# Performance work log

Measured on AMD Instinct MI355X. Metric: run time of the kernel, lower is better.

The kernel has to match this reference:

```python
import jax, jax.numpy as jnp
import numpy as np

B, H, L = 8, 256, 8192

def setup_inputs() -> dict:
    key = jax.random.key(0)
    k1, k2, k3 = jax.random.split(key, 3)
    u = jax.random.normal(k1, (B, H, L), dtype=jnp.float32)
    K = jax.random.normal(k2, (H, L), dtype=jnp.float32)
    # D ~ uniform_ring with min=max=1.0, field='real' -> random signs on unit ring
    D = jnp.where(jax.random.uniform(k3, (H,)) < 0.5, -1.0, 1.0).astype(jnp.float32)
    return {"u": u, "K": K, "D": D}

def reference(u, K, D):
    # FFT-based circular long convolution per channel: y = ifft(fft(u) * fft(K)).real
    u_s = jnp.fft.fft(u, axis=-1)            # (B,H,L) complex
    k_s = jnp.fft.fft(K, axis=-1)            # (H,L)   complex
    y = jnp.fft.ifft(u_s * k_s[None], axis=-1).real  # (B,H,L)
    y = y + D[None, :, None] * u             # skip connection D*u
    y = jnp.tanh(y)
    return y
```

## Files before the change

kernel.cpp:

```cpp
#include <hip/hip_runtime.h>
#include <math.h>


#define LL 8192
#define NT 256
#define HH 256
#define TWO_PI 6.2831853071795864f
#define CP16 0.980785280403230f
#define SP16 0.195090322016128f
#define CP8  0.92387953251129f
#define SP8  0.38268343236509f

__device__ __forceinline__ int PH(int e) { return e ^ ((e >> 4) & 15); }

__device__ __forceinline__ float fast_tanh(float x) {
    float e = __expf(2.0f * x);
    return 1.0f - 2.0f / (e + 1.0f);
}

template<int JT>
__device__ __forceinline__ void fill_pyr_cs(float c0, float s0, float Er, float Ei,
                                            float* twr, float* twi) {
    const int off = (1 << JT) - 1;
    twr[off] = c0; twi[off] = s0;
    #pragma unroll
    for (int m = 1; m < (1 << JT); ++m) {
        const float pr = twr[off + m - 1], pi = twi[off + m - 1];
        twr[off + m] = pr * Er - pi * Ei;
        twi[off + m] = pr * Ei + pi * Er;
    }
    #pragma unroll
    for (int j = JT - 1; j >= 0; --j) {
        #pragma unroll
        for (int m = 0; m < (1 << j); ++m) {
            const float a = twr[(2 << j) - 1 + m], b = twi[(2 << j) - 1 + m];
            twr[(1 << j) - 1 + m] = a * a - b * b;
            twi[(1 << j) - 1 + m] = 2.0f * a * b;
        }
    }
}
template<int JT>
__device__ __forceinline__ void fill_pyr(float ang0, float Er, float Ei,
                                         float* twr, float* twi) {
    float s, c;
    __sincosf(ang0, &s, &c);
    fill_pyr_cs<JT>(c, s, Er, Ei, twr, twi);
}

template<int R2>
__device__ __forceinline__ void dif_apply(float* xr, float* xi,
                                          const float* twr, const float* twi) {
    #pragma unroll
    for (int j = R2 - 1; j >= 0; --j) {
        #pragma unroll
        for (int q = 0; q < (1 << (R2 - 1)); ++q) {
            const int mm = q & ((1 << j) - 1);
            const int m0 = ((q >> j) << (j + 1)) | mm;
            const int m1 = m0 + (1 << j);
            const float wr = twr[(1 << j) - 1 + mm], wi = twi[(1 << j) - 1 + mm];
            const float ar = xr[m0], ai = xi[m0], br = xr[m1], bi = xi[m1];
            xr[m0] = ar + br; xi[m0] = ai + bi;
            const float dr = ar - br, di = ai - bi;
            xr[m1] = dr * wr - di * wi;
            xi[m1] = dr * wi + di * wr;
        }
    }
}
template<int R2>
__device__ __forceinline__ void dit_apply(float* xr, float* xi,
                                          const float* twr, const float* twi) {
    #pragma unroll
    for (int j = 0; j < R2; ++j) {
        #pragma unroll
        for (int q = 0; q < (1 << (R2 - 1)); ++q) {
            const int mm = q & ((1 << j) - 1);
            const int m0 = ((q >> j) << (j + 1)) | mm;
            const int m1 = m0 + (1 << j);
            const float wr = twr[(1 << j) - 1 + mm], wi = twi[(1 << j) - 1 + mm];
            const float br = xr[m1] * wr - xi[m1] * wi;
            const float bi = xr[m1] * wi + xi[m1] * wr;
            const float ar = xr[m0], ai = xi[m0];
            xr[m0] = ar + br; xi[m0] = ai + bi;
            xr[m1] = ar - br; xi[m1] = ai - bi;
        }
    }
}

__device__ __forceinline__ void fwd_A(float* xr, float* xi, int tid, float2* buf) {
    float twr[31], twi[31];
    fill_pyr<4>(-(TWO_PI / 8192.0f) * (float)tid, CP16, -SP16, twr, twi);
    dif_apply<5>(xr, xi, twr, twi);
    #pragma unroll
    for (int m = 0; m < 32; ++m) {
        buf[PH(tid + (m << 8))] = make_float2(xr[m], xi[m]);
    }
}

__device__ __forceinline__ void fwd_B(int tid, float2* buf) {
    int pa[2][16];
    float xr[2][16], xi[2][16], twr[15], twi[15];
    #pragma unroll
    for (int gg = 0; gg < 2; ++gg) {
        const int g = tid + (gg << 8);
        const int base = ((g >> 4) << 8) | (g & 15);
        #pragma unroll
        for (int m = 0; m < 16; ++m) {
            pa[gg][m] = PH(base + (m << 4));
            const float2 v = buf[pa[gg][m]];
            xr[gg][m] = v.x; xi[gg][m] = v.y;
        }
    }
    fill_pyr<3>(-(TWO_PI / 256.0f) * (float)(tid & 15), CP8, -SP8, twr, twi);
    dif_apply<4>(xr[0], xi[0], twr, twi);
    dif_apply<4>(xr[1], xi[1], twr, twi);
    #pragma unroll
    for (int gg = 0; gg < 2; ++gg) {
        #pragma unroll
        for (int m = 0; m < 16; ++m) {
            buf[pa[gg][m]] = make_float2(xr[gg][m], xi[gg][m]);
        }
    }
}

__device__ __forceinline__ void inv_B(int tid, float2* buf) {
    int pa[2][16];
    float xr[2][16], xi[2][16], twr[15], twi[15];
    #pragma unroll
    for (int gg = 0; gg < 2; ++gg) {
        const int g = tid + (gg << 8);
        const int base = ((g >> 4) << 8) | (g & 15);
        #pragma unroll
        for (int m = 0; m < 16; ++m) {
            pa[gg][m] = PH(base + (m << 4));
            const float2 v = buf[pa[gg][m]];
            xr[gg][m] = v.x; xi[gg][m] = v.y;
        }
    }
    fill_pyr<3>((TWO_PI / 256.0f) * (float)(tid & 15), CP8, SP8, twr, twi);
    dit_apply<4>(xr[0], xi[0], twr, twi);
    dit_apply<4>(xr[1], xi[1], twr, twi);
    #pragma unroll
    for (int gg = 0; gg < 2; ++gg) {
        #pragma unroll
        for (int m = 0; m < 16; ++m) {
            buf[pa[gg][m]] = make_float2(xr[gg][m], xi[gg][m]);
        }
    }
}

__global__ __launch_bounds__(NT) void kfft_kernel(const float* __restrict__ K,
                                                  const float* __restrict__ D,
                                                  float2* __restrict__ Kf) {
    __shared__ float2 buf[LL];
    const int h = blockIdx.x;
    const int tid = threadIdx.x;
    const float* Kr = K + (size_t)h * LL;
    float xr[32], xi[32];
    #pragma unroll
    for (int m = 0; m < 32; ++m) {
        xr[m] = Kr[tid + (m << 8)];
        xi[m] = 0.0f;
    }
    fwd_A(xr, xi, tid, buf);
    __syncthreads();
    fwd_B(tid, buf);
    __syncthreads();
    const float dh = D[h];
    const float invN = 1.0f / (float)LL;
    float2* outp = Kf + (size_t)h * LL;
    float twr[15], twi[15];
    fill_pyr_cs<3>(1.0f, 0.0f, CP8, -SP8, twr, twi);
    #pragma unroll
    for (int gg = 0; gg < 2; ++gg) {
        const int i0 = tid + (gg << 8);
        const int base = i0 << 4;
        float yr[16], yi[16];
        #pragma unroll
        for (int m = 0; m < 16; ++m) {
            const float2 v = buf[PH(base + m)];
            yr[m] = v.x; yi[m] = v.y;
        }
        dif_apply<4>(yr, yi, twr, twi);
        #pragma unroll
        for (int m = 0; m < 16; ++m) {
            outp[(m << 9) + i0] = make_float2((yr[m] + dh) * invN, yi[m] * invN);
        }
    }
}

__global__ __launch_bounds__(NT) void conv_kernel(const float* __restrict__ u,
                                                  const float2* __restrict__ Kf,
                                                  float* __restrict__ out) {
    __shared__ float2 buf[LL];
    const int tid = threadIdx.x;
    const int h = blockIdx.x & (HH - 1);
    const int pr_ = blockIdx.x >> 8;
    const size_t off0 = ((size_t)(pr_ * 2) * HH + h) * LL;
    const size_t off1 = off0 + (size_t)HH * LL;
    const float* u0 = u + off0;
    const float* u1 = u + off1;

    float xr[32], xi[32];
    #pragma unroll
    for (int m = 0; m < 32; ++m) {
        xr[m] = u0[tid + (m << 8)];
        xi[m] = u1[tid + (m << 8)];
    }
    fwd_A(xr, xi, tid, buf);
    __syncthreads();
    fwd_B(tid, buf);
    __syncthreads();

    {
        const float2* kf = Kf + (size_t)h * LL;
        int pc[2][16];
        float yr[2][16], yi[2][16], twr[15], twi[15];
        #pragma unroll
        for (int gg = 0; gg < 2; ++gg) {
            const int base = (tid + (gg << 8)) << 4;
            #pragma unroll
            for (int m = 0; m < 16; ++m) {
                pc[gg][m] = PH(base + m);
                const float2 v = buf[pc[gg][m]];
                yr[gg][m] = v.x; yi[gg][m] = v.y;
            }
        }
        fill_pyr_cs<3>(1.0f, 0.0f, CP8, -SP8, twr, twi);
        dif_apply<4>(yr[0], yi[0], twr, twi);
        dif_apply<4>(yr[1], yi[1], twr, twi);
        #pragma unroll
        for (int gg = 0; gg < 2; ++gg) {
            const int i0 = tid + (gg << 8);
            #pragma unroll
            for (int m = 0; m < 16; ++m) {
                const float2 w = kf[(m << 9) + i0];
                const float a = yr[gg][m], b = yi[gg][m];
                yr[gg][m] = a * w.x - b * w.y;
                yi[gg][m] = a * w.y + b * w.x;
            }
        }
        fill_pyr_cs<3>(1.0f, 0.0f, CP8, SP8, twr, twi);
        dit_apply<4>(yr[0], yi[0], twr, twi);
        dit_apply<4>(yr[1], yi[1], twr, twi);
        #pragma unroll
        for (int gg = 0; gg < 2; ++gg) {
            #pragma unroll
            for (int m = 0; m < 16; ++m) {
                buf[pc[gg][m]] = make_float2(yr[gg][m], yi[gg][m]);
            }
        }
    }
    __syncthreads();

    inv_B(tid, buf);
    __syncthreads();

    {
        float twr[31], twi[31];
        #pragma unroll
        for (int m = 0; m < 32; ++m) {
            const float2 v = buf[PH(tid + (m << 8))];
            xr[m] = v.x; xi[m] = v.y;
        }
        fill_pyr<4>((TWO_PI / 8192.0f) * (float)tid, CP16, SP16, twr, twi);
        dit_apply<5>(xr, xi, twr, twi);
    }
    float* o0 = out + off0;
    float* o1 = out + off1;
    #pragma unroll
    for (int m = 0; m < 32; ++m) {
        const int n = tid + (m << 8);
        o0[n] = fast_tanh(xr[m]);
        o1[n] = fast_tanh(xi[m]);
    }
}

extern "C" void kernel_launch(void* const* d_in, const int* in_sizes, int n_in,
                              void* d_out, int out_size, void* d_ws, size_t ws_size,
                              hipStream_t stream) {
    const float* u = (const float*)d_in[0];
    const float* K = (const float*)d_in[1];
    const float* D = (const float*)d_in[2];
    float* out = (float*)d_out;
    float2* Kf = (float2*)d_ws;

    kfft_kernel<<<dim3(HH), dim3(NT), 0, stream>>>(K, D, Kf);
    conv_kernel<<<dim3(4 * HH), dim3(NT), 0, stream>>>(u, Kf, out);
}
```

Before: 172.4 us.

## Fuse middle FFT stages per wavefront and split shared buffer into planar arrays

The middle radix-16 stages (forward B, the radix-16 C pass with pointwise multiply, and inverse B) are regrouped so each 16-lane group owns one 256-element column block. All of that work then stays inside a wavefront, and three block-wide __syncthreads between those stages are dropped. The shared buffer changes from interleaved float2 to separate real and imaginary arrays with a new XOR swizzle, which is meant to reduce bank conflicts. The frequency-domain kernel is now stored in natural contiguous order, so it is loaded as float4 and prefetched before the FFT stages. The risks are that the intra-wave shared-memory ordering relies on wavefront lockstep without explicit barriers, and that the prefetched kernel values add register pressure.

```diff
diff --git a/kernel.cpp b/kernel.cpp
--- a/kernel.cpp
+++ b/kernel.cpp
@@ -11,8 +11,9 @@
 #define CP8  0.92387953251129f
 #define SP8  0.38268343236509f
 
-__device__ __forceinline__ int PH(int e) { return e ^ ((e >> 4) & 15); }
-
+__device__ __forceinline__ int SW(int e) {
+    return e ^ ((e >> 4) & 15) ^ (((e >> 8) & 1) << 4);
+}
 __device__ __forceinline__ float fast_tanh(float x) {
     float e = __expf(2.0f * x);
     return 1.0f - 2.0f / (e + 1.0f);
@@ -86,72 +87,23 @@
     }
 }
 
-__device__ __forceinline__ void fwd_A(float* xr, float* xi, int tid, float2* buf) {
+__device__ __forceinline__ void fwd_A(float* xr, float* xi, int tid,
+                                      float* re, float* im) {
     float twr[31], twi[31];
     fill_pyr<4>(-(TWO_PI / 8192.0f) * (float)tid, CP16, -SP16, twr, twi);
     dif_apply<5>(xr, xi, twr, twi);
     #pragma unroll
     for (int m = 0; m < 32; ++m) {
-        buf[PH(tid + (m << 8))] = make_float2(xr[m], xi[m]);
-    }
-}
-
-__device__ __forceinline__ void fwd_B(int tid, float2* buf) {
-    int pa[2][16];
-    float xr[2][16], xi[2][16], twr[15], twi[15];
-    #pragma unroll
-    for (int gg = 0; gg < 2; ++gg) {
-        const int g = tid + (gg << 8);
-        const int base = ((g >> 4) << 8) | (g & 15);
-        #pragma unroll
-        for (int m = 0; m < 16; ++m) {
-            pa[gg][m] = PH(base + (m << 4));
-            const float2 v = buf[pa[gg][m]];
-            xr[gg][m] = v.x; xi[gg][m] = v.y;
-        }
-    }
-    fill_pyr<3>(-(TWO_PI / 256.0f) * (float)(tid & 15), CP8, -SP8, twr, twi);
-    dif_apply<4>(xr[0], xi[0], twr, twi);
-    dif_apply<4>(xr[1], xi[1], twr, twi);
-    #pragma unroll
-    for (int gg = 0; gg < 2; ++gg) {
-        #pragma unroll
-        for (int m = 0; m < 16; ++m) {
-            buf[pa[gg][m]] = make_float2(xr[gg][m], xi[gg][m]);
-        }
-    }
-}
-
-__device__ __forceinline__ void inv_B(int tid, float2* buf) {
-    int pa[2][16];
-    float xr[2][16], xi[2][16], twr[15], twi[15];
-    #pragma unroll
-    for (int gg = 0; gg < 2; ++gg) {
-        const int g = tid + (gg << 8);
-        const int base = ((g >> 4) << 8) | (g & 15);
-        #pragma unroll
-        for (int m = 0; m < 16; ++m) {
-            pa[gg][m] = PH(base + (m << 4));
-            const float2 v = buf[pa[gg][m]];
-            xr[gg][m] = v.x; xi[gg][m] = v.y;
-        }
-    }
-    fill_pyr<3>((TWO_PI / 256.0f) * (float)(tid & 15), CP8, SP8, twr, twi);
-    dit_apply<4>(xr[0], xi[0], twr, twi);
-    dit_apply<4>(xr[1], xi[1], twr, twi);
-    #pragma unroll
-    for (int gg = 0; gg < 2; ++gg) {
-        #pragma unroll
-        for (int m = 0; m < 16; ++m) {
-            buf[pa[gg][m]] = make_float2(xr[gg][m], xi[gg][m]);
-        }
+        const int p = SW(tid + (m << 8));
+        re[p] = xr[m]; im[p] = xi[m];
     }
 }
 
 __global__ __launch_bounds__(NT) void kfft_kernel(const float* __restrict__ K,
                                                   const float* __restrict__ D,
                                                   float2* __restrict__ Kf) {
-    __shared__ float2 buf[LL];
+    __shared__ float re[LL];
+    __shared__ float im[LL];
     const int h = blockIdx.x;
     const int tid = threadIdx.x;
     const float* Kr = K + (size_t)h * LL;
@@ -161,29 +113,57 @@
         xr[m] = Kr[tid + (m << 8)];
         xi[m] = 0.0f;
     }
-    fwd_A(xr, xi, tid, buf);
+    fwd_A(xr, xi, tid, re, im);
     __syncthreads();
-    fwd_B(tid, buf);
-    __syncthreads();
-    const float dh = D[h];
-    const float invN = 1.0f / (float)LL;
-    float2* outp = Kf + (size_t)h * LL;
-    float twr[15], twi[15];
-    fill_pyr_cs<3>(1.0f, 0.0f, CP8, -SP8, twr, twi);
-    #pragma unroll
-    for (int gg = 0; gg < 2; ++gg) {
-        const int i0 = tid + (gg << 8);
-        const int base = i0 << 4;
-        float yr[16], yi[16];
-        #pragma unroll
-        for (int m = 0; m < 16; ++m) {
-            const float2 v = buf[PH(base + m)];
-            yr[m] = v.x; yi[m] = v.y;
-        }
-        dif_apply<4>(yr, yi, twr, twi);
-        #pragma unroll
-        for (int m = 0; m < 16; ++m) {
-            outp[(m << 9) + i0] = make_float2((yr[m] + dh) * invN, yi[m] * invN);
+
+    const int lane = tid & 63, wv = tid >> 6;
+    const int q = lane & 15, qw = (lane >> 4) & 3;
+
+    {
+        float twr[15], twi[15];
+        fill_pyr<3>(-(TWO_PI / 256.0f) * (float)q, CP8, -SP8, twr, twi);
+        #pragma unroll
+        for (int r = 0; r < 2; ++r) {
+            const int c = (wv << 3) + qw + (r << 2);
+            const int base = (c << 8) + q;
+            float ar[16], ai[16];
+            #pragma unroll
+            for (int m = 0; m < 16; ++m) {
+                const int p = SW(base + (m << 4));
+                ar[m] = re[p]; ai[m] = im[p];
+            }
+            dif_apply<4>(ar, ai, twr, twi);
+            #pragma unroll
+            for (int m = 0; m < 16; ++m) {
+                const int p = SW(base + (m << 4));
+                re[p] = ar[m]; im[p] = ai[m];
+            }
+        }
+    }
+    {
+        const float dh = D[h];
+        const float invN = 1.0f / (float)LL;
+        float twr[15], twi[15];
+        fill_pyr_cs<3>(1.0f, 0.0f, CP8, -SP8, twr, twi);
+        #pragma unroll
+        for (int r = 0; r < 2; ++r) {
+            const int c = (wv << 3) + qw + (r << 2);
+            const int eb = (c << 8) + (q << 4);
+            float yr[16], yi[16];
+            #pragma unroll
+            for (int j = 0; j < 16; ++j) {
+                const int p = SW(eb + j);
+                yr[j] = re[p]; yi[j] = im[p];
+            }
+            dif_apply<4>(yr, yi, twr, twi);
+            float4* o4 = (float4*)(Kf + (size_t)h * LL + eb);
+            #pragma unroll
+            for (int jj = 0; jj < 8; ++jj) {
+                float4 v;
+                v.x = (yr[2 * jj]     + dh) * invN; v.y = yi[2 * jj]     * invN;
+                v.z = (yr[2 * jj + 1] + dh) * invN; v.w = yi[2 * jj + 1] * invN;
+                o4[jj] = v;
+            }
         }
     }
 }
@@ -191,7 +171,8 @@
 __global__ __launch_bounds__(NT) void conv_kernel(const float* __restrict__ u,
                                                   const float2* __restrict__ Kf,
                                                   float* __restrict__ out) {
-    __shared__ float2 buf[LL];
+    __shared__ float re[LL];
+    __shared__ float im[LL];
     const int tid = threadIdx.x;
     const int h = blockIdx.x & (HH - 1);
     const int pr_ = blockIdx.x >> 8;
@@ -206,61 +187,103 @@
         xr[m] = u0[tid + (m << 8)];
         xi[m] = u1[tid + (m << 8)];
     }
-    fwd_A(xr, xi, tid, buf);
+    fwd_A(xr, xi, tid, re, im);
     __syncthreads();
-    fwd_B(tid, buf);
+
+    const int lane = tid & 63, wv = tid >> 6;
+    const int q = lane & 15, qw = (lane >> 4) & 3;
+    const int c0 = (wv << 3) + qw;
+    const float2* kf = Kf + (size_t)h * LL;
+
+    float kwr[2][16], kwi[2][16];
+    #pragma unroll
+    for (int r = 0; r < 2; ++r) {
+        const int eb = ((c0 + (r << 2)) << 8) + (q << 4);
+        const float4* kp = (const float4*)(kf + eb);
+        #pragma unroll
+        for (int jj = 0; jj < 8; ++jj) {
+            const float4 v = kp[jj];
+            kwr[r][2 * jj] = v.x;     kwi[r][2 * jj] = v.y;
+            kwr[r][2 * jj + 1] = v.z; kwi[r][2 * jj + 1] = v.w;
+        }
+    }
+
+    {
+        float twr[15], twi[15];
+        fill_pyr<3>(-(TWO_PI / 256.0f) * (float)q, CP8, -SP8, twr, twi);
+        #pragma unroll
+        for (int r = 0; r < 2; ++r) {
+            const int base = ((c0 + (r << 2)) << 8) + q;
+            float ar[16], ai[16];
+            #pragma unroll
+            for (int m = 0; m < 16; ++m) {
+                const int p = SW(base + (m << 4));
+                ar[m] = re[p]; ai[m] = im[p];
+            }
+            dif_apply<4>(ar, ai, twr, twi);
+            #pragma unroll
+            for (int m = 0; m < 16; ++m) {
+                const int p = SW(base + (m << 4));
+                re[p] = ar[m]; im[p] = ai[m];
+            }
+        }
+    }
+    {
+        float twd_r[15], twd_i[15], twu_r[15], twu_i[15];
+        fill_pyr_cs<3>(1.0f, 0.0f, CP8, -SP8, twd_r, twd_i);
+        fill_pyr_cs<3>(1.0f, 0.0f, CP8, SP8, twu_r, twu_i);
+        #pragma unroll
+        for (int r = 0; r < 2; ++r) {
+            const int eb = ((c0 + (r << 2)) << 8) + (q << 4);
+            float yr[16], yi[16];
+            #pragma unroll
+            for (int j = 0; j < 16; ++j) {
+                const int p = SW(eb + j);
+                yr[j] = re[p]; yi[j] = im[p];
+            }
+            dif_apply<4>(yr, yi, twd_r, twd_i);
+            #pragma unroll
+            for (int j = 0; j < 16; ++j) {
+                const float a = yr[j], b = yi[j];
+                yr[j] = a * kwr[r][j] - b * kwi[r][j];
+                yi[j] = a * kwi[r][j] + b * kwr[r][j];
+            }
+            dit_apply<4>(yr, yi, twu_r, twu_i);
+            #pragma unroll
+            for (int j = 0; j < 16; ++j) {
+                const int p = SW(eb + j);
+                re[p] = yr[j]; im[p] = yi[j];
+            }
+        }
+    }
+    {
+        float twr[15], twi[15];
+        fill_pyr<3>((TWO_PI / 256.0f) * (float)q, CP8, SP8, twr, twi);
+        #pragma unroll
+        for (int r = 0; r < 2; ++r) {
+            const int base = ((c0 + (r << 2)) << 8) + q;
+            float ar[16], ai[16];
+            #pragma unroll
+            for (int m = 0; m < 16; ++m) {
+                const int p = SW(base + (m << 4));
+                ar[m] = re[p]; ai[m] = im[p];
+            }
+            dit_apply<4>(ar, ai, twr, twi);
+            #pragma unroll
+            for (int m = 0; m < 16; ++m) {
+                const int p = SW(base + (m << 4));
+                re[p] = ar[m]; im[p] = ai[m];
+            }
+        }
+    }
     __syncthreads();
 
     {
-        const float2* kf = Kf + (size_t)h * LL;
-        int pc[2][16];
-        float yr[2][16], yi[2][16], twr[15], twi[15];
-        #pragma unroll
-        for (int gg = 0; gg < 2; ++gg) {
-            const int base = (tid + (gg << 8)) << 4;
-            #pragma unroll
-            for (int m = 0; m < 16; ++m) {
-                pc[gg][m] = PH(base + m);
-                const float2 v = buf[pc[gg][m]];
-                yr[gg][m] = v.x; yi[gg][m] = v.y;
-            }
-        }
-        fill_pyr_cs<3>(1.0f, 0.0f, CP8, -SP8, twr, twi);
-        dif_apply<4>(yr[0], yi[0], twr, twi);
-        dif_apply<4>(yr[1], yi[1], twr, twi);
-        #pragma unroll
-        for (int gg = 0; gg < 2; ++gg) {
-            const int i0 = tid + (gg << 8);
-            #pragma unroll
-            for (int m = 0; m < 16; ++m) {
-                const float2 w = kf[(m << 9) + i0];
-                const float a = yr[gg][m], b = yi[gg][m];
-                yr[gg][m] = a * w.x - b * w.y;
-                yi[gg][m] = a * w.y + b * w.x;
-            }
-        }
-        fill_pyr_cs<3>(1.0f, 0.0f, CP8, SP8, twr, twi);
-        dit_apply<4>(yr[0], yi[0], twr, twi);
-        dit_apply<4>(yr[1], yi[1], twr, twi);
-        #pragma unroll
-        for (int gg = 0; gg < 2; ++gg) {
-            #pragma unroll
-            for (int m = 0; m < 16; ++m) {
-                buf[pc[gg][m]] = make_float2(yr[gg][m], yi[gg][m]);
-            }
-        }
-    }
-    __syncthreads();
-
-    inv_B(tid, buf);
-    __syncthreads();
-
-    {
         float twr[31], twi[31];
         #pragma unroll
         for (int m = 0; m < 32; ++m) {
-            const float2 v = buf[PH(tid + (m << 8))];
-            xr[m] = v.x; xi[m] = v.y;
+            const int p = SW(tid + (m << 8));
+            xr[m] = re[p]; xi[m] = im[p];
         }
         fill_pyr<4>((TWO_PI / 8192.0f) * (float)tid, CP16, SP16, twr, twi);
         dit_apply<5>(xr, xi, twr, twi);
```

After: 153.2 us. 11.2% less time.
